# Kernel tuning notes

Hardware: AMD Instinct MI355X
Metric: run time of the kernel (lower is better)

The kernel has to match this reference:

```python
import jax, jax.numpy as jnp
import numpy as np
import math

MAX_DISP = 4
STRIDE = 1
PAD = MAX_DISP


def setup_inputs() -> dict:
    key = jax.random.key(0)
    k1, k2 = jax.random.split(key)
    B, C, H, W = 8, 128, 128, 192
    x1 = jax.random.normal(k1, (B, C, H, W), dtype=jnp.float32)
    x2 = jax.random.normal(k2, (B, C, H, W), dtype=jnp.float32)
    return {"x1": x1, "x2": x2}


def reference(x1, x2):
    B, C, H, W = x1.shape
    inv_sqrt_c = np.float32(1.0 / math.sqrt(C))
    # zero-pad x2 spatially by max_displacement on each side
    x2p = jnp.pad(x2, ((0, 0), (0, 0), (PAD, PAD), (PAD, PAD)))
    corrs = []
    # fixed small loop over the 80 displacements (structural, unrolled under jit)
    for i in range(-MAX_DISP, MAX_DISP + 1, STRIDE):
        for j in range(-MAX_DISP, MAX_DISP + 1, STRIDE):
            if i == 0 and j == 0:
                continue
            x2_slice = x2p[:, :, PAD + i:PAD + i + H, PAD + j:PAD + j + W]
            # per-pixel dot product over channels, scaled by 1/sqrt(C)
            corrs.append(jnp.sum(x1 * x2_slice, axis=1) * inv_sqrt_c)
    # [B, 80, H, W]
    return jnp.stack(corrs, axis=1)
```

## Files before the change

kernel.cpp:

```cpp
#include <hip/hip_runtime.h>


#define B_  8
#define C_  128
#define H_  128
#define W_  192
#define HW_ (H_*W_)
#define WT  32
#define HT  8
#define NTHREADS 576

__device__ static const __attribute__((aligned(16))) float g_zero[4] = {0.f, 0.f, 0.f, 0.f};

__global__ __launch_bounds__(NTHREADS, 2) void corr_kernel(
    const float* __restrict__ x1, const float* __restrict__ x2,
    float* __restrict__ out)
{
    const int tx = threadIdx.x;
    const int ty = threadIdx.y;
    const int iz = threadIdx.z;

    const int bid = blockIdx.x;
    const int b   = bid & 7;
    const int t   = bid >> 3;
    const int w0t = (t % 6) * WT;
    const int h0t = (t / 6) * HT;

    const float* x1b = x1 + (size_t)b * C_ * HW_;
    const float* x2b = x2 + (size_t)b * C_ * HW_;

    const int h_out = h0t + ty;
    const int w_out = w0t + 4 * tx;

    const float* x1p = x1b + (size_t)h_out * W_ + w_out;

    const int r2 = h_out + iz - 4;
    const bool rowok = ((unsigned)r2 < (unsigned)H_);
    const int c0 = w_out - 4, c1 = w_out, c2 = w_out + 4;
    const bool ok0 = rowok && ((unsigned)c0 < (unsigned)W_);
    const bool ok1 = rowok;
    const bool ok2 = rowok && ((unsigned)c2 < (unsigned)W_);

    const float* zp = g_zero;
    const float* p0 = ok0 ? (x2b + (size_t)r2 * W_ + c0) : zp;
    const float* p1 = ok1 ? (x2b + (size_t)r2 * W_ + c1) : zp;
    const float* p2 = ok2 ? (x2b + (size_t)r2 * W_ + c2) : zp;
    const int s0 = ok0 ? HW_ : 0;
    const int s1 = ok1 ? HW_ : 0;
    const int s2 = ok2 ? HW_ : 0;

    float acc[9][4];
    #pragma unroll
    for (int j = 0; j < 9; j++)
        #pragma unroll
        for (int p = 0; p < 4; p++) acc[j][p] = 0.f;

    #pragma unroll 2
    for (int c = 0; c < C_; ++c) {
        const float4 a  = *(const float4*)(x1p);
        const float4 w0 = *(const float4*)(p0);
        const float4 w1 = *(const float4*)(p1);
        const float4 w2 = *(const float4*)(p2);
        x1p += HW_; p0 += s0; p1 += s1; p2 += s2;

        const float av[4] = {a.x, a.y, a.z, a.w};
        const float rr[12] = {w0.x, w0.y, w0.z, w0.w,
                              w1.x, w1.y, w1.z, w1.w,
                              w2.x, w2.y, w2.z, w2.w};
        #pragma unroll
        for (int j = 0; j < 9; j++)
            #pragma unroll
            for (int p = 0; p < 4; p++)
                acc[j][p] = fmaf(av[p], rr[j + p], acc[j][p]);
    }

    const float scale = 0.08838834764831845f;
    float* outb = out + (size_t)b * 80 * HW_ + (size_t)h_out * W_ + w_out;
    #pragma unroll
    for (int j = 0; j < 9; j++) {
        const int gi = iz * 9 + j;
        if (gi == 40) continue;
        const int ch = gi - (gi > 40 ? 1 : 0);
        float4 v;
        v.x = acc[j][0] * scale;
        v.y = acc[j][1] * scale;
        v.z = acc[j][2] * scale;
        v.w = acc[j][3] * scale;
        *(float4*)(outb + (size_t)ch * HW_) = v;
    }
}

extern "C" void kernel_launch(void* const* d_in, const int* in_sizes, int n_in,
                              void* d_out, int out_size, void* d_ws, size_t ws_size,
                              hipStream_t stream) {
    const float* x1 = (const float*)d_in[0];
    const float* x2 = (const float*)d_in[1];
    float* out = (float*)d_out;

    dim3 block(8, 8, 9);
    dim3 grid(768, 1, 1);
    corr_kernel<<<grid, block, 0, stream>>>(x1, x2, out);
}
```

Measured before the change: 496.4 us.

## Stage x2 halo tiles in double-buffered LDS and shrink per-thread output width

Each block now loads a haloed x2 tile (16 rows x 24 cols, 4 channels per chunk) into shared memory with register-prefetched double buffering. Threads read their shifted windows from LDS instead of issuing redundant global float4 loads. Per-thread work drops from 4 to 2 output pixels, the tile becomes 16 wide, and the grid doubles. This targets global and L2 traffic from overlapping x2 reads, at the cost of a block-wide barrier per chunk and a claimed occupancy of 7 blocks per CU.

```diff
diff --git a/kernel.cpp b/kernel.cpp
--- a/kernel.cpp
+++ b/kernel.cpp
@@ -6,72 +6,110 @@
 #define H_  128
 #define W_  192
 #define HW_ (H_*W_)
-#define WT  32
+#define HALO 4
+#define WT  16
 #define HT  8
+#define CC  4
+#define NCHUNK (C_/CC)
+#define X2C 24
+#define X2R 16
+#define X2SZ (X2R*X2C)
+#define BUFSZ (CC*X2SZ)
+#define NSLOT (BUFSZ/4)
 #define NTHREADS 576
 
-__device__ static const __attribute__((aligned(16))) float g_zero[4] = {0.f, 0.f, 0.f, 0.f};
-
-__global__ __launch_bounds__(NTHREADS, 2) void corr_kernel(
+__global__ __launch_bounds__(NTHREADS, 7) void corr_kernel(
     const float* __restrict__ x1, const float* __restrict__ x2,
     float* __restrict__ out)
 {
+    __shared__ float x2s[2][BUFSZ];
+
     const int tx = threadIdx.x;
     const int ty = threadIdx.y;
     const int iz = threadIdx.z;
+    const int tid = tx + 8*ty + 64*iz;
 
     const int bid = blockIdx.x;
     const int b   = bid & 7;
     const int t   = bid >> 3;
-    const int w0t = (t % 6) * WT;
-    const int h0t = (t / 6) * HT;
+    const int w0t = (t % 12) * WT;
+    const int h0t = (t / 12) * HT;
 
     const float* x1b = x1 + (size_t)b * C_ * HW_;
     const float* x2b = x2 + (size_t)b * C_ * HW_;
 
+    const bool stager = (tid < NSLOT);
+    const int e   = stager ? tid : 0;
+    const int ch0 = e / 96;
+    const int rem = e - 96*ch0;
+    const int r0  = rem / 6;
+    const int cq0 = rem - 6*r0;
+    const int gh0 = h0t - HALO + r0;
+    const int gw0 = w0t - HALO + 4*cq0;
+    const bool inb0 = stager && ((unsigned)gh0 < (unsigned)H_)
+                             && ((unsigned)gw0 < (unsigned)W_);
+    const int  l0   = 4 * e;
+    const float* ps0 = x2b + (inb0 ? ((long)ch0 * HW_ + (long)gh0 * W_ + gw0) : 0);
+    const long  st0 = inb0 ? (long)CC * HW_ : 0;
+
+    if (stager && !inb0) {
+        const float4 fz = make_float4(0.f, 0.f, 0.f, 0.f);
+        *(float4*)&x2s[0][l0] = fz;
+        *(float4*)&x2s[1][l0] = fz;
+    }
+
+    if (stager) {
+        const float4 t0 = *(const float4*)ps0;
+        if (inb0) *(float4*)&x2s[0][l0] = t0;
+    }
+    __syncthreads();
+
     const int h_out = h0t + ty;
-    const int w_out = w0t + 4 * tx;
+    const int w_out = w0t + 2 * tx;
+    const float* x1t = x1b + (size_t)h_out * W_ + w_out;
+    const int woff = (ty + iz) * X2C + 2 * tx;
 
-    const float* x1p = x1b + (size_t)h_out * W_ + w_out;
-
-    const int r2 = h_out + iz - 4;
-    const bool rowok = ((unsigned)r2 < (unsigned)H_);
-    const int c0 = w_out - 4, c1 = w_out, c2 = w_out + 4;
-    const bool ok0 = rowok && ((unsigned)c0 < (unsigned)W_);
-    const bool ok1 = rowok;
-    const bool ok2 = rowok && ((unsigned)c2 < (unsigned)W_);
-
-    const float* zp = g_zero;
-    const float* p0 = ok0 ? (x2b + (size_t)r2 * W_ + c0) : zp;
-    const float* p1 = ok1 ? (x2b + (size_t)r2 * W_ + c1) : zp;
-    const float* p2 = ok2 ? (x2b + (size_t)r2 * W_ + c2) : zp;
-    const int s0 = ok0 ? HW_ : 0;
-    const int s1 = ok1 ? HW_ : 0;
-    const int s2 = ok2 ? HW_ : 0;
-
-    float acc[9][4];
+    float acc[9][2];
     #pragma unroll
-    for (int j = 0; j < 9; j++)
-        #pragma unroll
-        for (int p = 0; p < 4; p++) acc[j][p] = 0.f;
+    for (int j = 0; j < 9; j++) { acc[j][0] = 0.f; acc[j][1] = 0.f; }
 
     #pragma unroll 2
-    for (int c = 0; c < C_; ++c) {
-        const float4 a  = *(const float4*)(x1p);
-        const float4 w0 = *(const float4*)(p0);
-        const float4 w1 = *(const float4*)(p1);
-        const float4 w2 = *(const float4*)(p2);
-        x1p += HW_; p0 += s0; p1 += s1; p2 += s2;
+    for (int k = 0; k < NCHUNK; ++k) {
+        const int cb = k * CC;
+        const bool more = (k + 1 < NCHUNK);
 
-        const float av[4] = {a.x, a.y, a.z, a.w};
-        const float rr[12] = {w0.x, w0.y, w0.z, w0.w,
-                              w1.x, w1.y, w1.z, w1.w,
-                              w2.x, w2.y, w2.z, w2.w};
+        float2 a[CC];
         #pragma unroll
-        for (int j = 0; j < 9; j++)
+        for (int cc = 0; cc < CC; ++cc)
+            a[cc] = *(const float2*)(x1t + (size_t)(cb + cc) * HW_);
+
+        float4 t0;
+        if (more && stager)
+            t0 = *(const float4*)(ps0 + (long)(k + 1) * st0);
+
+        const float* buf = &x2s[k & 1][0];
+        #pragma unroll
+        for (int cc = 0; cc < CC; ++cc) {
+            const float* row = buf + cc * X2SZ + woff;
+            const float2 w0 = *(const float2*)(row);
+            const float2 w1 = *(const float2*)(row + 2);
+            const float2 w2 = *(const float2*)(row + 4);
+            const float2 w3 = *(const float2*)(row + 6);
+            const float2 w4 = *(const float2*)(row + 8);
+            const float rr[10] = {w0.x, w0.y, w1.x, w1.y, w2.x,
+                                  w2.y, w3.x, w3.y, w4.x, w4.y};
+            const float ax = a[cc].x, ay = a[cc].y;
             #pragma unroll
-            for (int p = 0; p < 4; p++)
-                acc[j][p] = fmaf(av[p], rr[j + p], acc[j][p]);
+            for (int j = 0; j < 9; j++) {
+                acc[j][0] = fmaf(ax, rr[j],     acc[j][0]);
+                acc[j][1] = fmaf(ay, rr[j + 1], acc[j][1]);
+            }
+        }
+
+        if (more && inb0)
+            *(float4*)(&x2s[(k & 1) ^ 1][0] + l0) = t0;
+
+        __syncthreads();
     }
 
     const float scale = 0.08838834764831845f;
@@ -81,12 +119,10 @@
         const int gi = iz * 9 + j;
         if (gi == 40) continue;
         const int ch = gi - (gi > 40 ? 1 : 0);
-        float4 v;
+        float2 v;
         v.x = acc[j][0] * scale;
         v.y = acc[j][1] * scale;
-        v.z = acc[j][2] * scale;
-        v.w = acc[j][3] * scale;
-        *(float4*)(outb + (size_t)ch * HW_) = v;
+        *(float2*)(outb + (size_t)ch * HW_) = v;
     }
 }
 
@@ -98,6 +134,6 @@
     float* out = (float*)d_out;
 
     dim3 block(8, 8, 9);
-    dim3 grid(768, 1, 1);
+    dim3 grid(12 * 16 * 8, 1, 1);
     corr_kernel<<<grid, block, 0, stream>>>(x1, x2, out);
 }
```

After: 1.553 ms. 3.13x slower.
